# Optimization experiments

Measured on AMD Instinct MI355X. Metric: run time of the kernel, lower is better.

## Reference

```python
import jax, jax.numpy as jnp
import numpy as np


def _conv2d_same(x, w, b):
    # x: [B,H,W,Cin], w: [kh,kw,Cin,Cout] (Keras HWIO), b: [Cout]
    y = jax.lax.conv_general_dilated(
        x, w, window_strides=(1, 1), padding='SAME',
        dimension_numbers=('NHWC', 'HWIO', 'NHWC'))
    return y + b


def _bilateral_slice_apply(grid, guide, image):
    # HDRNet bilateral_slice_apply with has_offset=True.
    # grid:  [B, gh, gw, gd, (ci+1)*co]
    # guide: [B, H, W] in [0,1]
    # image: [B, H, W, ci]
    B, gh, gw, gd, nc = grid.shape
    _, H, W, ci = image.shape
    co = nc // (ci + 1)
    dt = grid.dtype

    # Continuous grid coordinates (HDRNet convention: pixel centers, -0.5 shift)
    gx = (jnp.arange(W, dtype=dt) + 0.5) * gw / W - 0.5          # [W]
    gy = (jnp.arange(H, dtype=dt) + 0.5) * gh / H - 0.5          # [H]
    gz = guide.astype(dt) * gd - 0.5                             # [B,H,W]

    fx = jnp.floor(gx)
    fy = jnp.floor(gy)
    fz = jnp.floor(gz)
    bidx = jnp.arange(B)[:, None, None]                          # [B,1,1]

    coeffs = jnp.zeros((B, H, W, nc), dtype=dt)
    for dz in (0, 1):
        zz = fz + dz
        wz = jnp.maximum(1.0 - jnp.abs(gz - zz), 0.0)            # [B,H,W]
        zi = jnp.clip(zz.astype(jnp.int32), 0, gd - 1)           # [B,H,W]
        for dy in (0, 1):
            yy = fy + dy
            wy = jnp.maximum(1.0 - jnp.abs(gy - yy), 0.0)        # [H]
            yi = jnp.clip(yy.astype(jnp.int32), 0, gh - 1)       # [H]
            for dx in (0, 1):
                xx = fx + dx
                wx = jnp.maximum(1.0 - jnp.abs(gx - xx), 0.0)    # [W]
                xi = jnp.clip(xx.astype(jnp.int32), 0, gw - 1)   # [W]
                corner = grid[bidx, yi[None, :, None], xi[None, None, :], zi]  # [B,H,W,nc]
                w = wz * wy[None, :, None] * wx[None, None, :]   # [B,H,W]
                coeffs = coeffs + corner * w[..., None]

    # Per-pixel affine transform: coeffs -> [B,H,W,co,ci+1]
    A = coeffs.reshape(B, H, W, co, ci + 1)
    return jnp.einsum('bhwoi,bhwi->bhwo', A[..., :ci], image) + A[..., ci]


def setup_inputs() -> dict:
    key = jax.random.key(0)
    k1, k2, k3, k4 = jax.random.split(key, 4)
    B, H, W = 4, 1024, 1024
    grid = jax.random.normal(k1, (B, 16, 16, 8, 12), dtype=jnp.float32)
    guide = jax.random.uniform(k2, (B, H, W), dtype=jnp.float32)
    image = jax.random.normal(k3, (B, H, W, 3), dtype=jnp.float32)
    conv_w = jax.random.normal(k4, (3, 3, 3, 3), dtype=jnp.float32) * 0.1
    conv_b = jnp.zeros((3,), dtype=jnp.float32)
    return {'grid': grid, 'guide': guide, 'image': image,
            'conv_w': conv_w, 'conv_b': conv_b}


def reference(grid, guide, image, conv_w, conv_b):
    x = _conv2d_same(image, conv_w, conv_b)
    return _bilateral_slice_apply(grid, guide, x)
```

## Files before the change

kernel.cpp:

```cpp
#include <hip/hip_runtime.h>

#define H_  1024
#define W_  1024
#define B_  4
#define GH  16
#define GW  16
#define GD  8
#define NC  12
#define CELLF (GD * NC)
#define YROWF (GW * CELLF)

#define TW 64
#define TH 8
#define LROWS (TH + 2)
#define LCOLS (TW + 2)
#define TABF (3 * CELLF)

typedef float f2 __attribute__((ext_vector_type(2)));

__global__ __launch_bounds__(256)
void fused_conv_slice(const float* __restrict__ grid,
                      const float* __restrict__ guide,
                      const float* __restrict__ image,
                      const float* __restrict__ conv_w,
                      const float* __restrict__ conv_b,
                      float* __restrict__ out)
{
    __shared__ float4 s_img4[LROWS][LCOLS];
    __shared__ __align__(16) float s_tab[TH][TABF];

    const int tx  = threadIdx.x;
    const int tyq = threadIdx.y;
    const int bx  = blockIdx.x;
    const int by  = blockIdx.y;
    const int b   = blockIdx.z;
    const int x0 = bx * TW;
    const int y0 = by * TH;
    const int tid = tyq * 64 + tx;
    const int imgbase = b * (H_ * W_ * 3);

    auto stage_px = [&](int rr, int c) {
        int yy = y0 - 1 + rr;
        int xx = x0 - 1 + c;
        float4 v = make_float4(0.f, 0.f, 0.f, 0.f);
        if (yy >= 0 && yy < H_ && xx >= 0 && xx < W_) {
            const float* p = image + imgbase + (yy * W_ + xx) * 3;
            v.x = p[0]; v.y = p[1]; v.z = p[2];
        }
        s_img4[rr][c] = v;
    };
    #pragma unroll
    for (int rr0 = 0; rr0 < LROWS; rr0 += 4) {
        int rr = rr0 + tyq;
        if (rr < LROWS) {
            stage_px(rr, tx);
            if (tx < 2) stage_px(rr, TW + tx);
        }
    }

    int cells[3];
    cells[0] = max(bx - 1, 0);
    cells[1] = bx;
    cells[2] = min(bx + 1, GW - 1);
    const float* gB = grid + b * (GH * GW * GD * NC);
    {
        int rr = tid >> 5;
        int le = tid & 31;
        int y  = y0 + rr;
        float gyf = (y + 0.5f) * (1.0f / 64.0f) - 0.5f;
        float fyf = floorf(gyf);
        float tyw = gyf - fyf;
        int iy = (int)fyf;
        int yi0 = min(max(iy, 0), GH - 1);
        int yi1 = min(max(iy + 1, 0), GH - 1);
        float wy0 = 1.0f - tyw, wy1 = tyw;
        const float2* G0 = (const float2*)(gB + yi0 * YROWF);
        const float2* G1 = (const float2*)(gB + yi1 * YROWF);
        float2* T = (float2*)&s_tab[rr][0];
        #pragma unroll
        for (int k = 0; k < 5; ++k) {
            int e = le + k * 32;
            if (e < 144) {
                int s = (e >= 96) ? 2 : ((e >= 48) ? 1 : 0);
                int re = e - s * 48;
                int off = cells[s] * 48 + re;
                float2 v0 = G0[off], v1 = G1[off];
                float2 w;
                w.x = wy0 * v0.x + wy1 * v1.x;
                w.y = wy0 * v0.y + wy1 * v1.y;
                T[e] = w;
            }
        }
    }

    const int x = x0 + tx;
    const int lr = tyq * 2;
    const int guidebase = b * (H_ * W_);
    float g2[2];
    #pragma unroll
    for (int j = 0; j < 2; ++j)
        g2[j] = guide[guidebase + (y0 + lr + j) * W_ + x];

    float wgt[81];
    #pragma unroll
    for (int i = 0; i < 81; ++i) wgt[i] = conv_w[i];
    float bias0 = conv_b[0], bias1 = conv_b[1], bias2 = conv_b[2];

    __syncthreads();

    float4 r0[3], r1[3], r2[3];
    float acc2r[2][3];

    auto loadrow = [&](int r, float4* d) {
        d[0] = s_img4[r][tx];
        d[1] = s_img4[r][tx + 1];
        d[2] = s_img4[r][tx + 2];
    };
    auto conv3 = [&](const float4* ra, const float4* rb, const float4* rc, float* acc) {
        acc[0] = bias0; acc[1] = bias1; acc[2] = bias2;
        const float4* rows[3] = {ra, rb, rc};
        #pragma unroll
        for (int kh = 0; kh < 3; ++kh)
            #pragma unroll
            for (int kw = 0; kw < 3; ++kw) {
                float4 v4 = rows[kh][kw];
                float v[3] = {v4.x, v4.y, v4.z};
                #pragma unroll
                for (int ci = 0; ci < 3; ++ci) {
                    int wb = ((kh * 3 + kw) * 3 + ci) * 3;
                    acc[0] += v[ci] * wgt[wb + 0];
                    acc[1] += v[ci] * wgt[wb + 1];
                    acc[2] += v[ci] * wgt[wb + 2];
                }
            }
    };

    loadrow(lr + 0, r0); loadrow(lr + 1, r1); loadrow(lr + 2, r2);
    conv3(r0, r1, r2, acc2r[0]);
    loadrow(lr + 3, r0);
    conv3(r1, r2, r0, acc2r[1]);

    float gxf = (x + 0.5f) * (1.0f / 64.0f) - 0.5f;
    float fxf = floorf(gxf);
    float txw = gxf - fxf;
    float wxa = 1.0f - txw, wxb = txw;
    int s0 = (int)fxf - (bx - 1);

    const int outbase = b * (H_ * W_ * 3);

    #pragma unroll
    for (int j = 0; j < 2; ++j) {
        int y = y0 + lr + j;
        const float* Tw = &s_tab[lr + j][0];

        float gzf = g2[j] * 8.0f - 0.5f;
        float fzf = floorf(gzf);
        float tz = gzf - fzf;
        int iz = (int)fzf;
        int zb = min(max(iz, 0), GD - 2);
        float wA = (iz < 0) ? 1.0f : ((iz > GD - 2) ? 0.0f : (1.0f - tz));
        float wB = 1.0f - wA;

        const float4* pA = (const float4*)(Tw + (s0 * GD + zb) * NC);
        const float4* pB = pA + 24;
        float m0 = wxa * wA, m1 = wxa * wB, m2 = wxb * wA, m3 = wxb * wB;
        f2 m0v = {m0, m0}, m1v = {m1, m1}, m2v = {m2, m2}, m3v = {m3, m3};

        float4 A0 = pA[0], A1 = pA[1], A2 = pA[2];
        float4 B0 = pA[3], B1 = pA[4], B2 = pA[5];
        float4 C0 = pB[0], C1 = pB[1], C2 = pB[2];
        float4 D0 = pB[3], D1 = pB[4], D2 = pB[5];

        f2 A[6] = {{A0.x,A0.y},{A0.z,A0.w},{A1.x,A1.y},{A1.z,A1.w},{A2.x,A2.y},{A2.z,A2.w}};
        f2 Bv[6] = {{B0.x,B0.y},{B0.z,B0.w},{B1.x,B1.y},{B1.z,B1.w},{B2.x,B2.y},{B2.z,B2.w}};
        f2 Cv[6] = {{C0.x,C0.y},{C0.z,C0.w},{C1.x,C1.y},{C1.z,C1.w},{C2.x,C2.y},{C2.z,C2.w}};
        f2 Dv[6] = {{D0.x,D0.y},{D0.z,D0.w},{D1.x,D1.y},{D1.z,D1.w},{D2.x,D2.y},{D2.z,D2.w}};
        f2 c[6];
        #pragma unroll
        for (int k = 0; k < 6; ++k)
            c[k] = __builtin_elementwise_fma(A[k], m0v,
                   __builtin_elementwise_fma(Bv[k], m1v,
                   __builtin_elementwise_fma(Cv[k], m2v, Dv[k] * m3v)));

        float a0 = acc2r[j][0], a1 = acc2r[j][1], a2 = acc2r[j][2];
        f2 q0 = {a0, a1}, q1 = {a2, 1.0f};
        f2 t0 = __builtin_elementwise_fma(c[0], q0, c[1] * q1);
        f2 t1 = __builtin_elementwise_fma(c[2], q0, c[3] * q1);
        f2 t2 = __builtin_elementwise_fma(c[4], q0, c[5] * q1);

        int oidx = outbase + (y * W_ + x) * 3;
        out[oidx + 0] = t0.x + t0.y;
        out[oidx + 1] = t1.x + t1.y;
        out[oidx + 2] = t2.x + t2.y;
    }
}

extern "C" void kernel_launch(void* const* d_in, const int* in_sizes, int n_in,
                              void* d_out, int out_size, void* d_ws, size_t ws_size,
                              hipStream_t stream) {
    const float* grid   = (const float*)d_in[0];
    const float* guide  = (const float*)d_in[1];
    const float* image  = (const float*)d_in[2];
    const float* conv_w = (const float*)d_in[3];
    const float* conv_b = (const float*)d_in[4];
    float* out = (float*)d_out;

    dim3 block(64, 4, 1);
    dim3 grid_dim(W_ / TW, H_ / TH, B_);
    fused_conv_slice<<<grid_dim, block, 0, stream>>>(grid, guide, image, conv_w, conv_b, out);
}
```

Baseline: 137.0 us.

## Store y-interpolated grid table in fp16 and slice with packed half math

New measurement: 135.5 us. Within noise of the previous version (-1.1%).

```diff
diff --git a/kernel.cpp b/kernel.cpp
--- a/kernel.cpp
+++ b/kernel.cpp
@@ -14,11 +14,13 @@
 #define TH 8
 #define LROWS (TH + 2)
 #define LCOLS (TW + 2)
-#define TABF (3 * CELLF)
-
-typedef float f2 __attribute__((ext_vector_type(2)));
-
-__global__ __launch_bounds__(256)
+#define TABH (3 * GD * 16)
+
+typedef _Float16 h2 __attribute__((ext_vector_type(2)));
+
+__device__ __forceinline__ h2 u2h(unsigned int u) { return __builtin_bit_cast(h2, u); }
+
+__global__ __launch_bounds__(256, 8)
 void fused_conv_slice(const float* __restrict__ grid,
                       const float* __restrict__ guide,
                       const float* __restrict__ image,
@@ -27,7 +29,7 @@
                       float* __restrict__ out)
 {
     __shared__ float4 s_img4[LROWS][LCOLS];
-    __shared__ __align__(16) float s_tab[TH][TABF];
+    __shared__ __align__(16) unsigned short s_tab[TH][TABH];
 
     const int tx  = threadIdx.x;
     const int tyq = threadIdx.y;
@@ -74,21 +76,27 @@
         int yi0 = min(max(iy, 0), GH - 1);
         int yi1 = min(max(iy + 1, 0), GH - 1);
         float wy0 = 1.0f - tyw, wy1 = tyw;
-        const float2* G0 = (const float2*)(gB + yi0 * YROWF);
-        const float2* G1 = (const float2*)(gB + yi1 * YROWF);
-        float2* T = (float2*)&s_tab[rr][0];
-        #pragma unroll
-        for (int k = 0; k < 5; ++k) {
+        const float4* G0 = (const float4*)(gB + yi0 * YROWF);
+        const float4* G1 = (const float4*)(gB + yi1 * YROWF);
+        #pragma unroll
+        for (int k = 0; k < 3; ++k) {
             int e = le + k * 32;
-            if (e < 144) {
-                int s = (e >= 96) ? 2 : ((e >= 48) ? 1 : 0);
-                int re = e - s * 48;
-                int off = cells[s] * 48 + re;
-                float2 v0 = G0[off], v1 = G1[off];
-                float2 w;
-                w.x = wy0 * v0.x + wy1 * v1.x;
-                w.y = wy0 * v0.y + wy1 * v1.y;
-                T[e] = w;
+            if (e < 72) {
+                int s  = (e >= 48) ? 2 : ((e >= 24) ? 1 : 0);
+                int re = e - s * 24;
+                int z  = re / 3;
+                int c4 = re - z * 3;
+                int off = cells[s] * 24 + re;
+                float4 v0 = G0[off], v1 = G1[off];
+                h2 p0, p1;
+                p0.x = (_Float16)(wy0 * v0.x + wy1 * v1.x);
+                p0.y = (_Float16)(wy0 * v0.y + wy1 * v1.y);
+                p1.x = (_Float16)(wy0 * v0.z + wy1 * v1.z);
+                p1.y = (_Float16)(wy0 * v0.w + wy1 * v1.w);
+                uint2 u;
+                u.x = __builtin_bit_cast(unsigned int, p0);
+                u.y = __builtin_bit_cast(unsigned int, p1);
+                *(uint2*)&s_tab[rr][(s * GD + z) * 16 + c4 * 4] = u;
             }
         }
     }
@@ -151,7 +159,7 @@
     #pragma unroll
     for (int j = 0; j < 2; ++j) {
         int y = y0 + lr + j;
-        const float* Tw = &s_tab[lr + j][0];
+        const unsigned short* Tr = &s_tab[lr + j][0];
 
         float gzf = g2[j] * 8.0f - 0.5f;
         float fzf = floorf(gzf);
@@ -161,37 +169,40 @@
         float wA = (iz < 0) ? 1.0f : ((iz > GD - 2) ? 0.0f : (1.0f - tz));
         float wB = 1.0f - wA;
 
-        const float4* pA = (const float4*)(Tw + (s0 * GD + zb) * NC);
-        const float4* pB = pA + 24;
         float m0 = wxa * wA, m1 = wxa * wB, m2 = wxb * wA, m3 = wxb * wB;
-        f2 m0v = {m0, m0}, m1v = {m1, m1}, m2v = {m2, m2}, m3v = {m3, m3};
-
-        float4 A0 = pA[0], A1 = pA[1], A2 = pA[2];
-        float4 B0 = pA[3], B1 = pA[4], B2 = pA[5];
-        float4 C0 = pB[0], C1 = pB[1], C2 = pB[2];
-        float4 D0 = pB[3], D1 = pB[4], D2 = pB[5];
-
-        f2 A[6] = {{A0.x,A0.y},{A0.z,A0.w},{A1.x,A1.y},{A1.z,A1.w},{A2.x,A2.y},{A2.z,A2.w}};
-        f2 Bv[6] = {{B0.x,B0.y},{B0.z,B0.w},{B1.x,B1.y},{B1.z,B1.w},{B2.x,B2.y},{B2.z,B2.w}};
-        f2 Cv[6] = {{C0.x,C0.y},{C0.z,C0.w},{C1.x,C1.y},{C1.z,C1.w},{C2.x,C2.y},{C2.z,C2.w}};
-        f2 Dv[6] = {{D0.x,D0.y},{D0.z,D0.w},{D1.x,D1.y},{D1.z,D1.w},{D2.x,D2.y},{D2.z,D2.w}};
-        f2 c[6];
+        h2 m0h = {(_Float16)m0, (_Float16)m0};
+        h2 m1h = {(_Float16)m1, (_Float16)m1};
+        h2 m2h = {(_Float16)m2, (_Float16)m2};
+        h2 m3h = {(_Float16)m3, (_Float16)m3};
+
+        const unsigned short* pA = Tr + (s0 * GD + zb) * 16;
+        uint4 Alo = *(const uint4*)(pA);            uint2 Ahi = *(const uint2*)(pA + 8);
+        uint4 Blo = *(const uint4*)(pA + 16);       uint2 Bhi = *(const uint2*)(pA + 24);
+        uint4 Clo = *(const uint4*)(pA + GD * 16);      uint2 Chi = *(const uint2*)(pA + GD * 16 + 8);
+        uint4 Dlo = *(const uint4*)(pA + GD * 16 + 16); uint2 Dhi = *(const uint2*)(pA + GD * 16 + 24);
+
+        h2 A[6] = {u2h(Alo.x), u2h(Alo.y), u2h(Alo.z), u2h(Alo.w), u2h(Ahi.x), u2h(Ahi.y)};
+        h2 Bv[6] = {u2h(Blo.x), u2h(Blo.y), u2h(Blo.z), u2h(Blo.w), u2h(Bhi.x), u2h(Bhi.y)};
+        h2 Cv[6] = {u2h(Clo.x), u2h(Clo.y), u2h(Clo.z), u2h(Clo.w), u2h(Chi.x), u2h(Chi.y)};
+        h2 Dv[6] = {u2h(Dlo.x), u2h(Dlo.y), u2h(Dlo.z), u2h(Dlo.w), u2h(Dhi.x), u2h(Dhi.y)};
+
+        h2 c[6];
         #pragma unroll
         for (int k = 0; k < 6; ++k)
-            c[k] = __builtin_elementwise_fma(A[k], m0v,
-                   __builtin_elementwise_fma(Bv[k], m1v,
-                   __builtin_elementwise_fma(Cv[k], m2v, Dv[k] * m3v)));
+            c[k] = __builtin_elementwise_fma(A[k], m0h,
+                   __builtin_elementwise_fma(Bv[k], m1h,
+                   __builtin_elementwise_fma(Cv[k], m2h, Dv[k] * m3h)));
 
         float a0 = acc2r[j][0], a1 = acc2r[j][1], a2 = acc2r[j][2];
-        f2 q0 = {a0, a1}, q1 = {a2, 1.0f};
-        f2 t0 = __builtin_elementwise_fma(c[0], q0, c[1] * q1);
-        f2 t1 = __builtin_elementwise_fma(c[2], q0, c[3] * q1);
-        f2 t2 = __builtin_elementwise_fma(c[4], q0, c[5] * q1);
+        h2 q01 = {(_Float16)a0, (_Float16)a1};
+        h2 q21 = {(_Float16)a2, (_Float16)1.0f};
 
         int oidx = outbase + (y * W_ + x) * 3;
-        out[oidx + 0] = t0.x + t0.y;
-        out[oidx + 1] = t1.x + t1.y;
-        out[oidx + 2] = t2.x + t2.y;
+        #pragma unroll
+        for (int o3 = 0; o3 < 3; ++o3) {
+            float t = __builtin_amdgcn_fdot2(c[2 * o3 + 1], q21, 0.0f, false);
+            out[oidx + o3] = __builtin_amdgcn_fdot2(c[2 * o3], q01, t, false);
+        }
     }
 }
 
```
